# Kernel tuning notes

Measured on AMD Instinct MI355X. Metric: run time of the kernel, lower is better.

Reference implementation:

```python
import jax, jax.numpy as jnp
import numpy as np

K = 500        # conv kernel == stride (non-overlapping windows)
C_IN = 8       # embedding dim
C_OUT = 128    # conv out channels
VOCAB = 257    # 256 byte values + padding idx 256


def setup_inputs() -> dict:
    key = jax.random.key(0)
    ks = jax.random.split(key, 10)
    B, L = 8, 1 << 20
    x = jax.random.randint(ks[0], (B, L), 0, VOCAB, dtype=jnp.int32)
    emb = 0.1 * jax.random.normal(ks[1], (VOCAB, C_IN), jnp.float32)
    emb = emb.at[VOCAB - 1].set(0.0)  # padding_idx=256 -> zero row
    lim_c = 1.0 / np.sqrt(C_IN * K)
    w1 = jax.random.uniform(ks[2], (C_OUT, C_IN, K), jnp.float32, -lim_c, lim_c)
    b1 = jax.random.uniform(ks[3], (C_OUT,), jnp.float32, -lim_c, lim_c)
    w2 = jax.random.uniform(ks[4], (C_OUT, C_IN, K), jnp.float32, -lim_c, lim_c)
    b2 = jax.random.uniform(ks[5], (C_OUT,), jnp.float32, -lim_c, lim_c)
    lim_d = 1.0 / np.sqrt(C_OUT)
    wd1 = jax.random.uniform(ks[6], (C_OUT, C_OUT), jnp.float32, -lim_d, lim_d)
    bd1 = jax.random.uniform(ks[7], (C_OUT,), jnp.float32, -lim_d, lim_d)
    wd2 = jax.random.uniform(ks[8], (1, C_OUT), jnp.float32, -lim_d, lim_d)
    bd2 = jax.random.uniform(ks[9], (1,), jnp.float32, -lim_d, lim_d)
    return {"x": x, "emb": emb, "w1": w1, "b1": b1, "w2": w2, "b2": b2,
            "wd1": wd1, "bd1": bd1, "wd2": wd2, "bd2": bd2}


def reference(x, emb, w1, b1, w2, b2, wd1, bd1, wd2, bd2):
    B, L = x.shape
    T = (L - K) // K + 1  # valid conv output length (== L // K here)
    xe = emb[x]                                  # [B, L, 8]  embedding lookup
    win = xe[:, : T * K].reshape(B, T, K, C_IN)  # [B, T, 500, 8] non-overlap windows
    c1 = jnp.einsum('btke,oek->bto', win, w1) + b1  # [B, T, 128]
    c2 = jnp.einsum('btke,oek->bto', win, w2) + b2
    gated = jax.nn.relu(c1) * jax.nn.sigmoid(c2)    # gated activation
    pooled = jnp.max(gated, axis=1)                 # global max pool over time -> [B, 128]
    h = jax.nn.relu(pooled @ wd1.T + bd1)           # [B, 128]
    out = jax.nn.sigmoid(h @ wd2.T + bd2)           # [B, 1]
    return out
```

## Files before the change

### kernel.cpp

```cpp
#include <hip/hip_runtime.h>

#define BATCH   8
#define LSEQ    1048576
#define KCONV   500
#define TWIN    2097
#define MROWS   16776
#define KDIM    4000
#define NDIM    256
#define COUT    128
#define VOCAB   257
#define VOCABP  256

#define BMR     80
#define NTILE   210
#define SLABP   20
#define NSLAB   25
#define NG      125
#define PLANE   (NDIM * 32)
#define AROWSH  168
#define STAGEN  (BMR * SLABP)

#define WTF_OFF   0ull
#define WTF_BYTES ((size_t)NG * PLANE * 2)
#define POOL_OFF  (WTF_OFF + WTF_BYTES)
#define CNT_OFF   (POOL_OFF + 4096)

typedef __attribute__((ext_vector_type(8))) __bf16 bf16x8;
typedef __attribute__((ext_vector_type(4))) float  floatx4;

__device__ inline unsigned short f2bf(float f) {
    union { float f; unsigned u; } c; c.f = f;
    return (unsigned short)((c.u + 0x7FFFu + ((c.u >> 16) & 1u)) >> 16);
}
__device__ inline unsigned pack2(float lo, float hi) {
    return (unsigned)f2bf(lo) | ((unsigned)f2bf(hi) << 16);
}

#define LDS_BARRIER() asm volatile("s_waitcnt lgkmcnt(0)\n\ts_barrier" ::: "memory")

__global__ __launch_bounds__(256) void wprep_kernel(const float* __restrict__ w1,
                                                    const float* __restrict__ w2,
                                                    unsigned short* __restrict__ Wtf,
                                                    float* __restrict__ pool,
                                                    int* __restrict__ cnt) {
    const int n   = blockIdx.x;
    const int tid = threadIdx.x;
    __shared__ float tile[KDIM];
    const float* src = (n < COUT) ? (w1 + (size_t)n * KDIM)
                                  : (w2 + (size_t)(n - COUT) * KDIM);
    for (int i = tid; i < KDIM; i += 256) tile[i] = src[i];
    __syncthreads();
    for (int i = tid; i < KDIM; i += 256) {
        int g = i >> 5, kk = i & 31;
        Wtf[(size_t)g * PLANE + n * 32 + kk] = f2bf(tile[(i & 7) * KCONV + (i >> 3)]);
    }
    if (n == 0) {
        if (tid < 256) ((float4*)pool)[tid] = float4{0.f, 0.f, 0.f, 0.f};
        if (tid == 0) *cnt = 0;
    }
}

__global__ __launch_bounds__(512) void gemm_kernel(const int* __restrict__ x,
                                                   const float* __restrict__ emb,
                                                   const unsigned short* __restrict__ Wtf,
                                                   const float* __restrict__ b1,
                                                   const float* __restrict__ b2,
                                                   float* __restrict__ pool,
                                                   int* __restrict__ cnt,
                                                   const float* __restrict__ wd1,
                                                   const float* __restrict__ bd1,
                                                   const float* __restrict__ wd2,
                                                   const float* __restrict__ bd2,
                                                   float* __restrict__ out) {
    __shared__ unsigned short tableL[VOCAB * 8];
    __shared__ unsigned short As[2][BMR * AROWSH];

    const int tid  = threadIdx.x;
    const int lane = tid & 63;
    const int wv   = tid >> 6;
    const int m0   = blockIdx.x * BMR;
    const int r16  = lane & 15;
    const int q    = lane >> 4;

    if (tid < VOCAB) {
        const float4* er = (const float4*)(emb + tid * 8);
        float4 a = er[0], b = er[1];
        uint4 u;
        u.x = pack2(a.x, a.y); u.y = pack2(a.z, a.w);
        u.z = pack2(b.x, b.y); u.w = pack2(b.z, b.w);
        *(uint4*)(tableL + tid * 8) = u;
    }

    const int* xptr[4];
    int        loff[4];
    bool       sval[4];
#pragma unroll
    for (int l = 0; l < 4; ++l) {
        int idx = tid + 512 * l;
        sval[l] = (idx < STAGEN);
        int ic  = sval[l] ? idx : 0;
        int row = ic / SLABP;
        int pos = ic - row * SLABP;
        int am  = m0 + row;
        bool av = sval[l] && (am < MROWS);
        sval[l] = av;
        int amc = av ? am : 0;
        int b   = amc / TWIN;
        int t   = amc - b * TWIN;
        xptr[l] = x + ((size_t)b * LSEQ + (size_t)t * KCONV + pos);
        loff[l] = row * AROWSH + pos * 8;
    }

    const int o = wv * 16 + r16;
    const size_t boff0 = (size_t)o * 32 + q * 8;
    const size_t boff1 = (size_t)(o + 128) * 32 + q * 8;

    floatx4 acc[5][2];
#pragma unroll
    for (int i = 0; i < 5; ++i) { acc[i][0] = floatx4{0,0,0,0}; acc[i][1] = floatx4{0,0,0,0}; }

    int xv[4], xn[4];
#pragma unroll
    for (int l = 0; l < 4; ++l) xv[l] = sval[l] ? xptr[l][0] : VOCABP;
    __syncthreads();

#pragma unroll
    for (int l = 0; l < 4; ++l) {
        if (l == 3 && tid >= STAGEN - 3 * 512) break;
        uint4 g = *(const uint4*)(tableL + xv[l] * 8);
        *(uint4*)((unsigned short*)As + loff[l]) = g;
    }
#pragma unroll
    for (int l = 0; l < 4; ++l) xv[l] = sval[l] ? xptr[l][SLABP] : VOCABP;
    LDS_BARRIER();

    bf16x8 bc0[2], bc1[2], bc2[2] = {};
    bc0[0] = *(const bf16x8*)(Wtf + boff0);
    bc0[1] = *(const bf16x8*)(Wtf + boff1);
    bc1[0] = *(const bf16x8*)(Wtf + PLANE + boff0);
    bc1[1] = *(const bf16x8*)(Wtf + PLANE + boff1);

    int buf = 0;
    for (int s = 0; s < NSLAB; ++s) {
        if (s + 2 < NSLAB) {
#pragma unroll
            for (int l = 0; l < 4; ++l)
                xn[l] = sval[l] ? xptr[l][(s + 2) * SLABP] : VOCABP;
        }

        const unsigned short* Asb = (const unsigned short*)As + buf * (BMR * AROWSH);
#pragma unroll
        for (int kt = 0; kt < 5; ++kt) {
            const int g = s * 5 + kt;
            if (g + 2 < NG) {
                const unsigned short* Wp = Wtf + (size_t)(g + 2) * PLANE;
                bc2[0] = *(const bf16x8*)(Wp + boff0);
                bc2[1] = *(const bf16x8*)(Wp + boff1);
            }
            bf16x8 af[5];
#pragma unroll
            for (int i = 0; i < 5; ++i)
                af[i] = *(const bf16x8*)(Asb + (i * 16 + r16) * AROWSH + (kt * 4 + q) * 8);
#pragma unroll
            for (int i = 0; i < 5; ++i) {
                acc[i][0] = __builtin_amdgcn_mfma_f32_16x16x32_bf16(af[i], bc0[0], acc[i][0], 0, 0, 0);
                acc[i][1] = __builtin_amdgcn_mfma_f32_16x16x32_bf16(af[i], bc0[1], acc[i][1], 0, 0, 0);
            }
            bc0[0] = bc1[0]; bc0[1] = bc1[1];
            bc1[0] = bc2[0]; bc1[1] = bc2[1];
        }

        if (s + 1 < NSLAB) {
            unsigned short* d = (unsigned short*)As + (buf ^ 1) * (BMR * AROWSH);
#pragma unroll
            for (int l = 0; l < 4; ++l) {
                if (l == 3 && tid >= STAGEN - 3 * 512) break;
                uint4 g = *(const uint4*)(tableL + xv[l] * 8);
                *(uint4*)(d + loff[l]) = g;
            }
        }
#pragma unroll
        for (int l = 0; l < 4; ++l) xv[l] = xn[l];
        LDS_BARRIER();
        buf ^= 1;
    }

    const float b1v = b1[o], b2v = b2[o];
    float cur = 0.0f;
    int curb  = (m0 + q * 4) / TWIN;
#pragma unroll
    for (int i = 0; i < 5; ++i) {
#pragma unroll
        for (int rg = 0; rg < 4; ++rg) {
            const int row = m0 + i * 16 + q * 4 + rg;
            if (row < MROWS) {
                const int bb = row / TWIN;
                if (bb != curb) {
                    atomicMax((int*)&pool[curb * COUT + o], __float_as_int(cur));
                    cur = 0.0f; curb = bb;
                }
                const float c1 = acc[i][0][rg] + b1v;
                const float c2 = acc[i][1][rg] + b2v;
                const float g  = fmaxf(c1, 0.0f) / (1.0f + __expf(-c2));
                cur = fmaxf(cur, g);
            }
        }
    }
    atomicMax((int*)&pool[curb * COUT + o], __float_as_int(cur));

    asm volatile("s_waitcnt vmcnt(0)" ::: "memory");
    __syncthreads();
    __shared__ int lastFlag;
    if (tid == 0) {
        int prev = __hip_atomic_fetch_add(cnt, 1, __ATOMIC_RELAXED, __HIP_MEMORY_SCOPE_AGENT);
        lastFlag = (prev == NTILE - 1) ? 1 : 0;
    }
    __syncthreads();
    if (!lastFlag) return;

    float* poolL = (float*)As;
    float* red   = poolL + BATCH * COUT;
    poolL[tid] = __int_as_float(
        __hip_atomic_load((int*)&pool[tid], __ATOMIC_RELAXED, __HIP_MEMORY_SCOPE_AGENT));
    poolL[tid + 512] = __int_as_float(
        __hip_atomic_load((int*)&pool[tid + 512], __ATOMIC_RELAXED, __HIP_MEMORY_SCOPE_AGENT));
    __syncthreads();

    if (tid < COUT) {
        const int j = tid;
        const float wj = wd2[j];
#pragma unroll
        for (int b = 0; b < BATCH; ++b) {
            float s = bd1[j];
            for (int i = 0; i < COUT; ++i) s += poolL[b * COUT + i] * wd1[j * COUT + i];
            red[b * COUT + j] = fmaxf(s, 0.0f) * wj;
        }
    }
    __syncthreads();
    if (tid < BATCH) {
        float s = 0.0f;
        for (int i = 0; i < COUT; ++i) s += red[tid * COUT + i];
        out[tid] = 1.0f / (1.0f + expf(-(s + bd2[0])));
    }
}

extern "C" void kernel_launch(void* const* d_in, const int* in_sizes, int n_in,
                              void* d_out, int out_size, void* d_ws, size_t ws_size,
                              hipStream_t stream) {
    const int*   x   = (const int*)d_in[0];
    const float* emb = (const float*)d_in[1];
    const float* w1  = (const float*)d_in[2];
    const float* b1  = (const float*)d_in[3];
    const float* w2  = (const float*)d_in[4];
    const float* b2  = (const float*)d_in[5];
    const float* wd1 = (const float*)d_in[6];
    const float* bd1 = (const float*)d_in[7];
    const float* wd2 = (const float*)d_in[8];
    const float* bd2 = (const float*)d_in[9];
    float* out = (float*)d_out;

    unsigned short* Wtf  = (unsigned short*)((char*)d_ws + WTF_OFF);
    float*          pool = (float*)((char*)d_ws + POOL_OFF);
    int*            cnt  = (int*)((char*)d_ws + CNT_OFF);

    wprep_kernel<<<dim3(NDIM), dim3(256), 0, stream>>>(w1, w2, Wtf, pool, cnt);
    gemm_kernel<<<dim3(NTILE), dim3(512), 0, stream>>>(x, emb, Wtf, b1, b2, pool, cnt,
                                                       wd1, bd1, wd2, bd2, out);
}
```

Baseline: 168.2 us.

## Pad embedding LDS table and interleave gather staging with MFMA k-steps

```diff
diff --git a/kernel.cpp b/kernel.cpp
--- a/kernel.cpp
+++ b/kernel.cpp
@@ -19,6 +19,7 @@
 #define PLANE   (NDIM * 32)
 #define AROWSH  168
 #define STAGEN  (BMR * SLABP)
+#define TSTRIDE 18
 
 #define WTF_OFF   0ull
 #define WTF_BYTES ((size_t)NG * PLANE * 2)
@@ -72,8 +73,8 @@
                                                    const float* __restrict__ wd2,
                                                    const float* __restrict__ bd2,
                                                    float* __restrict__ out) {
-    __shared__ unsigned short tableL[VOCAB * 8];
-    __shared__ unsigned short As[2][BMR * AROWSH];
+    __shared__ __align__(16) unsigned short tableL[VOCAB * TSTRIDE];
+    __shared__ __align__(16) unsigned short As[2][BMR * AROWSH];
 
     const int tid  = threadIdx.x;
     const int lane = tid & 63;
@@ -85,17 +86,18 @@
     if (tid < VOCAB) {
         const float4* er = (const float4*)(emb + tid * 8);
         float4 a = er[0], b = er[1];
-        uint4 u;
-        u.x = pack2(a.x, a.y); u.y = pack2(a.z, a.w);
-        u.z = pack2(b.x, b.y); u.w = pack2(b.z, b.w);
-        *(uint4*)(tableL + tid * 8) = u;
+        unsigned* tb = (unsigned*)(tableL + tid * TSTRIDE);
+        tb[0] = pack2(a.x, a.y); tb[1] = pack2(a.z, a.w);
+        tb[2] = pack2(b.x, b.y); tb[3] = pack2(b.z, b.w);
     }
 
     const int* xptr[4];
     int        loff[4];
     bool       sval[4];
+    bool       sact[4];
 #pragma unroll
     for (int l = 0; l < 4; ++l) {
+        sact[l] = (l < 3) || (tid < STAGEN - 3 * 512);
         int idx = tid + 512 * l;
         sval[l] = (idx < STAGEN);
         int ic  = sval[l] ? idx : 0;
@@ -126,9 +128,11 @@
 
 #pragma unroll
     for (int l = 0; l < 4; ++l) {
-        if (l == 3 && tid >= STAGEN - 3 * 512) break;
-        uint4 g = *(const uint4*)(tableL + xv[l] * 8);
-        *(uint4*)((unsigned short*)As + loff[l]) = g;
+        if (sact[l]) {
+            const unsigned* gb = (const unsigned*)(tableL + xv[l] * TSTRIDE);
+            uint4 g; g.x = gb[0]; g.y = gb[1]; g.z = gb[2]; g.w = gb[3];
+            *(uint4*)((unsigned short*)As + loff[l]) = g;
+        }
     }
 #pragma unroll
     for (int l = 0; l < 4; ++l) xv[l] = sval[l] ? xptr[l][SLABP] : VOCABP;
@@ -148,7 +152,11 @@
                 xn[l] = sval[l] ? xptr[l][(s + 2) * SLABP] : VOCABP;
         }
 
-        const unsigned short* Asb = (const unsigned short*)As + buf * (BMR * AROWSH);
+        const unsigned short* Asb  = (const unsigned short*)As + buf * (BMR * AROWSH);
+        unsigned short*       dstS = (unsigned short*)As + (buf ^ 1) * (BMR * AROWSH);
+        const bool stg = (s + 1 < NSLAB);
+        uint4 gr[4];
+
 #pragma unroll
         for (int kt = 0; kt < 5; ++kt) {
             const int g = s * 5 + kt;
@@ -161,6 +169,12 @@
 #pragma unroll
             for (int i = 0; i < 5; ++i)
                 af[i] = *(const bf16x8*)(Asb + (i * 16 + r16) * AROWSH + (kt * 4 + q) * 8);
+
+            if (kt < 4 && stg && sact[kt]) {
+                const unsigned* gb = (const unsigned*)(tableL + xv[kt] * TSTRIDE);
+                gr[kt].x = gb[0]; gr[kt].y = gb[1]; gr[kt].z = gb[2]; gr[kt].w = gb[3];
+            }
+
 #pragma unroll
             for (int i = 0; i < 5; ++i) {
                 acc[i][0] = __builtin_amdgcn_mfma_f32_16x16x32_bf16(af[i], bc0[0], acc[i][0], 0, 0, 0);
@@ -168,16 +182,9 @@
             }
             bc0[0] = bc1[0]; bc0[1] = bc1[1];
             bc1[0] = bc2[0]; bc1[1] = bc2[1];
-        }
-
-        if (s + 1 < NSLAB) {
-            unsigned short* d = (unsigned short*)As + (buf ^ 1) * (BMR * AROWSH);
-#pragma unroll
-            for (int l = 0; l < 4; ++l) {
-                if (l == 3 && tid >= STAGEN - 3 * 512) break;
-                uint4 g = *(const uint4*)(tableL + xv[l] * 8);
-                *(uint4*)(d + loff[l]) = g;
-            }
+
+            if (kt >= 1 && stg && sact[kt - 1])
+                *(uint4*)(dstS + loff[kt - 1]) = gr[kt - 1];
         }
 #pragma unroll
         for (int l = 0; l < 4; ++l) xv[l] = xn[l];
```

Result: faster. 161.1 us (-4.2%).
